# Kernel tuning notes

Hardware: AMD Instinct MI355X
Metric: run time of the kernel (lower is better)

## Reference

```python
import jax, jax.numpy as jnp
import numpy as np

N_VEH, N_PED = 16, 16
DV, DP = 40, 24            # vehicle / pedestrian slot obs dims
N = N_VEH + N_PED          # 32 agents
E, H = 128, 4              # embed_dim, num_heads
DH = E // H                # head_dim = 32
B = 4096
OBS = N_VEH * DV + N_PED * DP + N  # 1056


def setup_inputs() -> dict:
    key = jax.random.key(0)
    ks = jax.random.split(key, 12)
    s = lambda fan_in: 1.0 / np.sqrt(fan_in)
    inp = {
        "global_obs": jax.random.uniform(ks[0], (B, OBS), dtype=jnp.float32),
        # per-type projectors (stored as (in, out) so x @ W + b)
        "Wv": jax.random.uniform(ks[1], (DV, E), jnp.float32, -s(DV), s(DV)),
        "bv": jax.random.uniform(ks[2], (E,), jnp.float32, -s(DV), s(DV)),
        "Wp": jax.random.uniform(ks[3], (DP, E), jnp.float32, -s(DP), s(DP)),
        "bp": jax.random.uniform(ks[4], (E,), jnp.float32, -s(DP), s(DP)),
        # GAT layer 0 / 1: w (E, H*DH), a_src / a_dst (H, DH)
        "w0": jax.random.normal(ks[5], (E, H * DH), jnp.float32) * s(E),
        "asrc0": jax.random.normal(ks[6], (H, DH), jnp.float32) * s(DH),
        "adst0": jax.random.normal(ks[7], (H, DH), jnp.float32) * s(DH),
        "w1": jax.random.normal(ks[8], (E, H * DH), jnp.float32) * s(E),
        "asrc1": jax.random.normal(ks[9], (H, DH), jnp.float32) * s(DH),
        "adst1": jax.random.normal(ks[10], (H, DH), jnp.float32) * s(DH),
    }
    return inp


def _gat(x, alive, w, a_src, a_dst):
    # x: (B,N,E), alive: (B,N) in {0,1}
    b, n, _ = x.shape
    h = (x @ w).reshape(b, n, H, DH)                       # (B,N,H,DH)
    alpha_src = jnp.einsum("bnhd,hd->bnh", h, a_src)       # (B,N,H)
    alpha_dst = jnp.einsum("bnhd,hd->bnh", h, a_dst)
    e = alpha_src[:, :, None, :] + alpha_dst[:, None, :, :]  # (B,Ni,Nj,H)
    e = jnp.where(e > 0, e, 0.2 * e)                       # LeakyReLU(0.2)
    key_mask = alive[:, None, :, None] >= 0.5              # mask over j
    e = jnp.where(key_mask, e, -jnp.inf)
    attn = jax.nn.softmax(e, axis=2)                       # softmax over keys j
    attn = jnp.nan_to_num(attn)
    out = jnp.einsum("bijh,bjhd->bihd", attn, h)           # weighted aggregate
    return out.reshape(b, n, H * DH)                       # concat heads


def reference(global_obs, Wv, bv, Wp, bp, w0, asrc0, adst0, w1, asrc1, adst1):
    b = global_obs.shape[0]
    veh = global_obs[:, : N_VEH * DV].reshape(b, N_VEH, DV)
    ped = global_obs[:, N_VEH * DV : N_VEH * DV + N_PED * DP].reshape(b, N_PED, DP)
    alive_raw = global_obs[:, -N:]
    tokens = jnp.concatenate([veh @ Wv + bv, ped @ Wp + bp], axis=1)  # (B,N,E)
    alive = (alive_raw >= 0.5).astype(jnp.float32)
    all_dead = jnp.sum(alive, axis=1, keepdims=True) < 0.5
    alive = jnp.where(all_dead, jnp.ones_like(alive), alive)
    x = tokens
    for (w, a_s, a_d) in ((w0, asrc0, adst0), (w1, asrc1, adst1)):
        x = jax.nn.elu(_gat(x, alive, w, a_s, a_d))
    aw = alive[:, :, None]
    pooled = jnp.sum(x * aw, axis=1) / jnp.clip(jnp.sum(aw, axis=1), 1.0)
    return pooled
```

## Files before the change

kernel.cpp:

```cpp
#include <hip/hip_runtime.h>


#define NTOK 32
#define EMB  128
#define OBSL 1056
#define XSTR 136

typedef __attribute__((ext_vector_type(8))) short  short8;
typedef __attribute__((ext_vector_type(4))) float  floatx4;
typedef __attribute__((ext_vector_type(2))) unsigned uint2v;

__device__ __forceinline__ short f2bf(float f) {
  union { float f; unsigned u; } v; v.f = f;
  unsigned r = (v.u + 0x7fffu + ((v.u >> 16) & 1u)) >> 16;
  return (short)(unsigned short)r;
}
__device__ __forceinline__ unsigned pk2(float a, float b) {
  unsigned r; asm("v_cvt_pk_bf16_f32 %0, %1, %2" : "=v"(r) : "v"(a), "v"(b)); return r;
}
__device__ __forceinline__ float exp2_hw(float x) {
#if __has_builtin(__builtin_amdgcn_exp2f)
  return __builtin_amdgcn_exp2f(x);
#else
  return exp2f(x);
#endif
}
__device__ __forceinline__ float rcp_hw(float x) {
#if __has_builtin(__builtin_amdgcn_rcpf)
  return __builtin_amdgcn_rcpf(x);
#else
  return 1.0f / x;
#endif
}
__device__ __forceinline__ float elu1(float v) { return v > 0.f ? v : __expf(v) - 1.f; }
__device__ __forceinline__ floatx4 mfma16(short8 a, short8 b, floatx4 c) {
  return __builtin_amdgcn_mfma_f32_16x16x32_bf16(a, b, c, 0, 0, 0);
}

__global__ void prep_weights(const float* __restrict__ Wv, const float* __restrict__ Wp,
                             const float* __restrict__ w0, const float* __restrict__ w1,
                             short* __restrict__ ws) {
  int idx = blockIdx.x * 256 + threadIdx.x;
  if (idx < 8192) {
    int e = idx >> 6, k = idx & 63;
    float v = (k < 40) ? Wv[(size_t)k * EMB + e] : Wp[(size_t)(k - 40) * EMB + e];
    ws[idx] = f2bf(v);
  } else if (idx < 24576) {
    int t = idx - 8192; int e = t >> 7, k = t & 127;
    ws[idx] = f2bf(w0[(size_t)k * EMB + e]);
  } else {
    int t = idx - 24576; int e = t >> 7, k = t & 127;
    ws[idx] = f2bf(w1[(size_t)k * EMB + e]);
  }
}

__global__ __launch_bounds__(256, 4) void gnn_fused(
    const float* __restrict__ obs,
    const float* __restrict__ bv, const float* __restrict__ bp,
    const float* __restrict__ as0, const float* __restrict__ ad0,
    const float* __restrict__ as1, const float* __restrict__ ad1,
    const short* __restrict__ wsb,
    float* __restrict__ out)
{
  __shared__ __align__(16) short s_xh[EMB * XSTR];
  __shared__ float s_pool[4 * EMB];

  const int tid  = threadIdx.x;
  const int lane = tid & 63;
  const int wv   = tid >> 6;
  const int col  = lane & 15;
  const int quad = lane >> 4;
  const int b    = blockIdx.x * 4 + wv;

  const float* orow = obs + (size_t)b * OBSL;
  short* xbase = &s_xh[(wv * NTOK) * XSTR];
  const short8  z8 = {0,0,0,0,0,0,0,0};
  const floatx4 fz = {0.f,0.f,0.f,0.f};

  float flag; float invc;
  {
    float araw = (lane < NTOK) ? orow[1024 + lane] : 0.f;
    bool alv = (lane < NTOK) && (araw >= 0.5f);
    unsigned long long m = __ballot(alv);
    int cnt = __popcll(m);
    flag = alv ? 1.f : 0.f;
    if (cnt == 0) { flag = (lane < NTOK) ? 1.f : 0.f; cnt = NTOK; }
    invc = 1.f / (float)cnt;
  }
  float alv8[8];
  #pragma unroll
  for (int jj = 0; jj < 8; ++jj) alv8[jj] = __shfl(flag, quad * 8 + jj);
  const float alvI0 = __shfl(flag, col);
  const float alvI1 = __shfl(flag, 16 + col);

  #pragma unroll
  for (int it = 0; it < 4; ++it) {
    int c = it * 64 + lane;
    *(short8*)&xbase[(c >> 3) * XSTR + (c & 7) * 8] = z8;
  }
  #pragma unroll
  for (int it = 0; it < 4; ++it) {
    int i4 = it * 64 + lane;
    float4 v = *(const float4*)&orow[i4 * 4];
    int r, k;
    if (i4 < 160) { r = (i4 * 205) >> 11;  k = (i4 - r * 10) * 4; }
    else { int t2 = i4 - 160; int q6 = (t2 * 171) >> 10; r = 16 + q6; k = 40 + (t2 - q6 * 6) * 4; }
    uint2v u; u.x = pk2(v.x, v.y); u.y = pk2(v.z, v.w);
    *(uint2v*)&xbase[r * XSTR + k] = u;
  }

  {
    short8 Bxin[2][2];
    #pragma unroll
    for (int nt = 0; nt < 2; ++nt)
      #pragma unroll
      for (int kt = 0; kt < 2; ++kt)
        Bxin[nt][kt] = *(const short8*)&xbase[(nt * 16 + col) * XSTR + kt * 32 + quad * 8];
    const short* embT = wsb;
    #pragma unroll
    for (int mtE = 0; mtE < 8; ++mtE) {
      short8 A0 = *(const short8*)&embT[(mtE * 16 + col) * 64 + quad * 8];
      short8 A1 = *(const short8*)&embT[(mtE * 16 + col) * 64 + 32 + quad * 8];
      float4 bv4 = *(const float4*)&bv[mtE * 16 + quad * 4];
      float4 bp4 = *(const float4*)&bp[mtE * 16 + quad * 4];
      #pragma unroll
      for (int nt = 0; nt < 2; ++nt) {
        floatx4 acc = fz;
        acc = mfma16(A0, Bxin[nt][0], acc);
        acc = mfma16(A1, Bxin[nt][1], acc);
        float4 bb = nt ? bp4 : bv4;
        uint2v u; u.x = pk2(acc[0] + bb.x, acc[1] + bb.y); u.y = pk2(acc[2] + bb.z, acc[3] + bb.w);
        *(uint2v*)&xbase[(nt * 16 + col) * XSTR + mtE * 16 + quad * 4] = u;
      }
    }
  }

  for (int L = 0; L < 2; ++L) {
    const short* wT  = wsb + 8192 + L * 16384;
    const float* gas = L ? as1 : as0;
    const float* gad = L ? ad1 : ad0;

    short8 Bx[4][2];
    #pragma unroll
    for (int kt = 0; kt < 4; ++kt)
      #pragma unroll
      for (int nt = 0; nt < 2; ++nt)
        Bx[kt][nt] = *(const short8*)&xbase[(nt * 16 + col) * XSTR + kt * 32 + quad * 8];
    __syncthreads();

    float psrc[4][2], pdst[4][2];
    #pragma unroll
    for (int hh = 0; hh < 4; ++hh) { psrc[hh][0]=0.f; psrc[hh][1]=0.f; pdst[hh][0]=0.f; pdst[hh][1]=0.f; }
    #pragma unroll
    for (int g = 0; g < 2; ++g) {
      floatx4 acc[4][2];
      #pragma unroll
      for (int mi = 0; mi < 4; ++mi) { acc[mi][0] = fz; acc[mi][1] = fz; }
      #pragma unroll
      for (int mi = 0; mi < 4; ++mi) {
        const int mt = g * 4 + mi;
        const short* wrow = &wT[(mt * 16 + col) * 128 + quad * 8];
        short8 A0 = *(const short8*)&wrow[0];
        short8 A1 = *(const short8*)&wrow[32];
        short8 A2 = *(const short8*)&wrow[64];
        short8 A3 = *(const short8*)&wrow[96];
        #pragma unroll
        for (int nt = 0; nt < 2; ++nt) {
          acc[mi][nt] = mfma16(A0, Bx[0][nt], acc[mi][nt]);
          acc[mi][nt] = mfma16(A1, Bx[1][nt], acc[mi][nt]);
          acc[mi][nt] = mfma16(A2, Bx[2][nt], acc[mi][nt]);
          acc[mi][nt] = mfma16(A3, Bx[3][nt], acc[mi][nt]);
        }
      }
      #pragma unroll
      for (int mi = 0; mi < 4; ++mi) {
        const int mt = g * 4 + mi;
        const int hh = mt >> 1;
        float4 cs = *(const float4*)&gas[mt * 16 + quad * 4];
        float4 cd = *(const float4*)&gad[mt * 16 + quad * 4];
        #pragma unroll
        for (int nt = 0; nt < 2; ++nt) {
          floatx4 a = acc[mi][nt];
          psrc[hh][nt] += a[0]*cs.x + a[1]*cs.y + a[2]*cs.z + a[3]*cs.w;
          pdst[hh][nt] += a[0]*cd.x + a[1]*cd.y + a[2]*cd.z + a[3]*cd.w;
          unsigned u01 = pk2(a[0], a[1]);
          unsigned u23 = pk2(a[2], a[3]);
          unsigned short* hrow = (unsigned short*)&s_xh[(mt * 16 + quad * 4) * XSTR + wv * NTOK + nt * 16 + col];
          hrow[0]        = (unsigned short)u01;
          hrow[XSTR]     = (unsigned short)(u01 >> 16);
          hrow[2 * XSTR] = (unsigned short)u23;
          hrow[3 * XSTR] = (unsigned short)(u23 >> 16);
        }
      }
    }

    #pragma unroll
    for (int hh = 0; hh < 4; ++hh)
      #pragma unroll
      for (int nt = 0; nt < 2; ++nt) {
        float vs = psrc[hh][nt]; vs += __shfl_xor(vs, 16); vs += __shfl_xor(vs, 32);
        psrc[hh][nt] = vs * 1.44269504088896340736f;
        float vd = pdst[hh][nt]; vd += __shfl_xor(vd, 16); vd += __shfl_xor(vd, 32);
        pdst[hh][nt] = vd * 1.44269504088896340736f;
      }

    short8 pf[4][2];
    #pragma unroll
    for (int hh = 0; hh < 4; ++hh) {
      float vsel = (quad >> 1) ? pdst[hh][1] : pdst[hh][0];
      float ad8[8];
      #pragma unroll
      for (int jj = 0; jj < 8; ++jj) {
        float v = __shfl(vsel, ((quad >> 1) << 5) + ((quad & 1) << 3) + jj);
        ad8[jj] = (alv8[jj] >= 0.5f) ? v : -1e30f;
      }
      #pragma unroll
      for (int ii = 0; ii < 2; ++ii) {
        float ai = psrc[hh][ii];
        float ev[8]; float sum = 0.f;
        #pragma unroll
        for (int jj = 0; jj < 8; ++jj) {
          float e = ai + ad8[jj];
          e = fmaxf(e, 0.2f * e);
          float p = exp2_hw(e);
          ev[jj] = p; sum += p;
        }
        sum += __shfl_xor(sum, 16);
        sum += __shfl_xor(sum, 32);
        float inv = rcp_hw(sum);
        union { unsigned u4[4]; short8 s; } pu;
        #pragma unroll
        for (int p2 = 0; p2 < 4; ++p2) pu.u4[p2] = pk2(ev[2*p2] * inv, ev[2*p2+1] * inv);
        pf[hh][ii] = pu.s;
      }
    }

    short8 Ah[4][2];
    #pragma unroll
    for (int hh = 0; hh < 4; ++hh)
      #pragma unroll
      for (int mtE = 0; mtE < 2; ++mtE)
        Ah[hh][mtE] = *(const short8*)&s_xh[(hh * 32 + mtE * 16 + col) * XSTR + wv * NTOK + quad * 8];
    if (L == 0) __syncthreads();

    #pragma unroll
    for (int hh = 0; hh < 4; ++hh)
      #pragma unroll
      for (int mtE = 0; mtE < 2; ++mtE) {
        floatx4 po[2];
        #pragma unroll
        for (int nt = 0; nt < 2; ++nt) {
          po[nt] = mfma16(Ah[hh][mtE], pf[hh][nt], fz);
        }
        if (L == 0) {
          #pragma unroll
          for (int nt = 0; nt < 2; ++nt) {
            uint2v u;
            u.x = pk2(elu1(po[nt][0]), elu1(po[nt][1]));
            u.y = pk2(elu1(po[nt][2]), elu1(po[nt][3]));
            *(uint2v*)&xbase[(nt * 16 + col) * XSTR + hh * 32 + mtE * 16 + quad * 4] = u;
          }
        } else {
          #pragma unroll
          for (int r = 0; r < 4; ++r) {
            float s = elu1(po[0][r]) * alvI0 + elu1(po[1][r]) * alvI1;
            s += __shfl_xor(s, 1); s += __shfl_xor(s, 2);
            s += __shfl_xor(s, 4); s += __shfl_xor(s, 8);
            if (col == 0) s_pool[wv * EMB + hh * 32 + mtE * 16 + quad * 4 + r] = s;
          }
        }
      }
  }

  float r0 = s_pool[wv * EMB + lane];
  float r1 = s_pool[wv * EMB + 64 + lane];
  out[(size_t)b * EMB + lane]      = r0 * invc;
  out[(size_t)b * EMB + 64 + lane] = r1 * invc;
}

extern "C" void kernel_launch(void* const* d_in, const int* in_sizes, int n_in,
                              void* d_out, int out_size, void* d_ws, size_t ws_size,
                              hipStream_t stream) {
  const float* obs = (const float*)d_in[0];
  const float* Wv  = (const float*)d_in[1];
  const float* bv  = (const float*)d_in[2];
  const float* Wp  = (const float*)d_in[3];
  const float* bp  = (const float*)d_in[4];
  const float* w0  = (const float*)d_in[5];
  const float* as0 = (const float*)d_in[6];
  const float* ad0 = (const float*)d_in[7];
  const float* w1  = (const float*)d_in[8];
  const float* as1 = (const float*)d_in[9];
  const float* ad1 = (const float*)d_in[10];
  float* out = (float*)d_out;
  short* wsb = (short*)d_ws;

  int Bn = in_sizes[0] / OBSL;
  prep_weights<<<160, 256, 0, stream>>>(Wv, Wp, w0, w1, wsb);
  gnn_fused<<<Bn / 4, 256, 0, stream>>>(obs, bv, bp, as0, ad0, as1, ad1, wsb, out);
}
```

Baseline: 141.1 us.

## Split each batch item across two waves by head pairs and shrink LDS

Each batch item is now handled by two waves, and each wave computes two of the four attention heads. A block now covers two items instead of four, and the launch grid doubles. The per-wave h tile uses a compact stride in a smaller shared buffer, and launch bounds are raised to allow 8 blocks per CU for higher occupancy and lower per-wave latency. Pooled results are written straight to global memory from lane 0 of each group, which removes the s_pool staging. In exchange, extra block-wide barriers are needed to coordinate the two waves that share an item's x tile.

```diff
diff --git a/kernel.cpp b/kernel.cpp
--- a/kernel.cpp
+++ b/kernel.cpp
@@ -5,6 +5,8 @@
 #define EMB  128
 #define OBSL 1056
 #define XSTR 136
+#define HSTR 40
+#define TILE 5120
 
 typedef __attribute__((ext_vector_type(8))) short  short8;
 typedef __attribute__((ext_vector_type(4))) float  floatx4;
@@ -54,7 +56,7 @@
   }
 }
 
-__global__ __launch_bounds__(256, 4) void gnn_fused(
+__global__ __launch_bounds__(256, 8) void gnn_fused(
     const float* __restrict__ obs,
     const float* __restrict__ bv, const float* __restrict__ bp,
     const float* __restrict__ as0, const float* __restrict__ ad0,
@@ -62,18 +64,20 @@
     const short* __restrict__ wsb,
     float* __restrict__ out)
 {
-  __shared__ __align__(16) short s_xh[EMB * XSTR];
-  __shared__ float s_pool[4 * EMB];
+  __shared__ __align__(16) short s_t[2][TILE];
 
   const int tid  = threadIdx.x;
   const int lane = tid & 63;
   const int wv   = tid >> 6;
+  const int item = wv >> 1;
+  const int hw   = wv & 1;
   const int col  = lane & 15;
   const int quad = lane >> 4;
-  const int b    = blockIdx.x * 4 + wv;
+  const int b    = blockIdx.x * 2 + item;
 
   const float* orow = obs + (size_t)b * OBSL;
-  short* xbase = &s_xh[(wv * NTOK) * XSTR];
+  short* xbase = s_t[item];
+  short* hbase = &s_t[item][hw * 2560];
   const short8  z8 = {0,0,0,0,0,0,0,0};
   const floatx4 fz = {0.f,0.f,0.f,0.f};
 
@@ -87,20 +91,18 @@
     if (cnt == 0) { flag = (lane < NTOK) ? 1.f : 0.f; cnt = NTOK; }
     invc = 1.f / (float)cnt;
   }
-  float alv8[8];
-  #pragma unroll
-  for (int jj = 0; jj < 8; ++jj) alv8[jj] = __shfl(flag, quad * 8 + jj);
   const float alvI0 = __shfl(flag, col);
   const float alvI1 = __shfl(flag, 16 + col);
 
   #pragma unroll
-  for (int it = 0; it < 4; ++it) {
-    int c = it * 64 + lane;
+  for (int it = 0; it < 2; ++it) {
+    int c = (hw * 2 + it) * 64 + lane;
     *(short8*)&xbase[(c >> 3) * XSTR + (c & 7) * 8] = z8;
   }
+  __syncthreads();
   #pragma unroll
-  for (int it = 0; it < 4; ++it) {
-    int i4 = it * 64 + lane;
+  for (int it = 0; it < 2; ++it) {
+    int i4 = (hw * 2 + it) * 64 + lane;
     float4 v = *(const float4*)&orow[i4 * 4];
     int r, k;
     if (i4 < 160) { r = (i4 * 205) >> 11;  k = (i4 - r * 10) * 4; }
@@ -108,6 +110,7 @@
     uint2v u; u.x = pk2(v.x, v.y); u.y = pk2(v.z, v.w);
     *(uint2v*)&xbase[r * XSTR + k] = u;
   }
+  __syncthreads();
 
   {
     short8 Bxin[2][2];
@@ -116,9 +119,11 @@
       #pragma unroll
       for (int kt = 0; kt < 2; ++kt)
         Bxin[nt][kt] = *(const short8*)&xbase[(nt * 16 + col) * XSTR + kt * 32 + quad * 8];
+    __syncthreads();
     const short* embT = wsb;
     #pragma unroll
-    for (int mtE = 0; mtE < 8; ++mtE) {
+    for (int mi = 0; mi < 4; ++mi) {
+      const int mtE = hw * 4 + mi;
       short8 A0 = *(const short8*)&embT[(mtE * 16 + col) * 64 + quad * 8];
       short8 A1 = *(const short8*)&embT[(mtE * 16 + col) * 64 + 32 + quad * 8];
       float4 bv4 = *(const float4*)&bv[mtE * 16 + quad * 4];
@@ -140,6 +145,8 @@
     const float* gas = L ? as1 : as0;
     const float* gad = L ? ad1 : ad0;
 
+    __syncthreads();
+
     short8 Bx[4][2];
     #pragma unroll
     for (int kt = 0; kt < 4; ++kt)
@@ -148,17 +155,17 @@
         Bx[kt][nt] = *(const short8*)&xbase[(nt * 16 + col) * XSTR + kt * 32 + quad * 8];
     __syncthreads();
 
-    float psrc[4][2], pdst[4][2];
-    #pragma unroll
-    for (int hh = 0; hh < 4; ++hh) { psrc[hh][0]=0.f; psrc[hh][1]=0.f; pdst[hh][0]=0.f; pdst[hh][1]=0.f; }
+    float psrc[2][2], pdst[2][2];
+    #pragma unroll
+    for (int hl = 0; hl < 2; ++hl) { psrc[hl][0]=0.f; psrc[hl][1]=0.f; pdst[hl][0]=0.f; pdst[hl][1]=0.f; }
     #pragma unroll
     for (int g = 0; g < 2; ++g) {
-      floatx4 acc[4][2];
-      #pragma unroll
-      for (int mi = 0; mi < 4; ++mi) { acc[mi][0] = fz; acc[mi][1] = fz; }
-      #pragma unroll
-      for (int mi = 0; mi < 4; ++mi) {
-        const int mt = g * 4 + mi;
+      floatx4 acc[2][2];
+      #pragma unroll
+      for (int mi = 0; mi < 2; ++mi) { acc[mi][0] = fz; acc[mi][1] = fz; }
+      #pragma unroll
+      for (int mi = 0; mi < 2; ++mi) {
+        const int mt = hw * 4 + g * 2 + mi;
         const short* wrow = &wT[(mt * 16 + col) * 128 + quad * 8];
         short8 A0 = *(const short8*)&wrow[0];
         short8 A1 = *(const short8*)&wrow[32];
@@ -173,41 +180,45 @@
         }
       }
       #pragma unroll
-      for (int mi = 0; mi < 4; ++mi) {
-        const int mt = g * 4 + mi;
-        const int hh = mt >> 1;
+      for (int mi = 0; mi < 2; ++mi) {
+        const int mt = hw * 4 + g * 2 + mi;
         float4 cs = *(const float4*)&gas[mt * 16 + quad * 4];
         float4 cd = *(const float4*)&gad[mt * 16 + quad * 4];
+        const int rowloc = (g * 2 + mi) * 16 + quad * 4;
         #pragma unroll
         for (int nt = 0; nt < 2; ++nt) {
           floatx4 a = acc[mi][nt];
-          psrc[hh][nt] += a[0]*cs.x + a[1]*cs.y + a[2]*cs.z + a[3]*cs.w;
-          pdst[hh][nt] += a[0]*cd.x + a[1]*cd.y + a[2]*cd.z + a[3]*cd.w;
+          psrc[g][nt] += a[0]*cs.x + a[1]*cs.y + a[2]*cs.z + a[3]*cs.w;
+          pdst[g][nt] += a[0]*cd.x + a[1]*cd.y + a[2]*cd.z + a[3]*cd.w;
           unsigned u01 = pk2(a[0], a[1]);
           unsigned u23 = pk2(a[2], a[3]);
-          unsigned short* hrow = (unsigned short*)&s_xh[(mt * 16 + quad * 4) * XSTR + wv * NTOK + nt * 16 + col];
+          unsigned short* hrow = (unsigned short*)&hbase[rowloc * HSTR + nt * 16 + col];
           hrow[0]        = (unsigned short)u01;
-          hrow[XSTR]     = (unsigned short)(u01 >> 16);
-          hrow[2 * XSTR] = (unsigned short)u23;
-          hrow[3 * XSTR] = (unsigned short)(u23 >> 16);
+          hrow[HSTR]     = (unsigned short)(u01 >> 16);
+          hrow[2 * HSTR] = (unsigned short)u23;
+          hrow[3 * HSTR] = (unsigned short)(u23 >> 16);
         }
       }
     }
 
     #pragma unroll
-    for (int hh = 0; hh < 4; ++hh)
+    for (int hl = 0; hl < 2; ++hl)
       #pragma unroll
       for (int nt = 0; nt < 2; ++nt) {
-        float vs = psrc[hh][nt]; vs += __shfl_xor(vs, 16); vs += __shfl_xor(vs, 32);
-        psrc[hh][nt] = vs * 1.44269504088896340736f;
-        float vd = pdst[hh][nt]; vd += __shfl_xor(vd, 16); vd += __shfl_xor(vd, 32);
-        pdst[hh][nt] = vd * 1.44269504088896340736f;
-      }
-
-    short8 pf[4][2];
-    #pragma unroll
-    for (int hh = 0; hh < 4; ++hh) {
-      float vsel = (quad >> 1) ? pdst[hh][1] : pdst[hh][0];
+        float vs = psrc[hl][nt]; vs += __shfl_xor(vs, 16); vs += __shfl_xor(vs, 32);
+        psrc[hl][nt] = vs * 1.44269504088896340736f;
+        float vd = pdst[hl][nt]; vd += __shfl_xor(vd, 16); vd += __shfl_xor(vd, 32);
+        pdst[hl][nt] = vd * 1.44269504088896340736f;
+      }
+
+    float alv8[8];
+    #pragma unroll
+    for (int jj = 0; jj < 8; ++jj) alv8[jj] = __shfl(flag, quad * 8 + jj);
+
+    short8 pf[2][2];
+    #pragma unroll
+    for (int hl = 0; hl < 2; ++hl) {
+      float vsel = (quad >> 1) ? pdst[hl][1] : pdst[hl][0];
       float ad8[8];
       #pragma unroll
       for (int jj = 0; jj < 8; ++jj) {
@@ -216,7 +227,7 @@
       }
       #pragma unroll
       for (int ii = 0; ii < 2; ++ii) {
-        float ai = psrc[hh][ii];
+        float ai = psrc[hl][ii];
         float ev[8]; float sum = 0.f;
         #pragma unroll
         for (int jj = 0; jj < 8; ++jj) {
@@ -231,34 +242,35 @@
         union { unsigned u4[4]; short8 s; } pu;
         #pragma unroll
         for (int p2 = 0; p2 < 4; ++p2) pu.u4[p2] = pk2(ev[2*p2] * inv, ev[2*p2+1] * inv);
-        pf[hh][ii] = pu.s;
+        pf[hl][ii] = pu.s;
       }
     }
 
-    short8 Ah[4][2];
-    #pragma unroll
-    for (int hh = 0; hh < 4; ++hh)
-      #pragma unroll
-      for (int mtE = 0; mtE < 2; ++mtE)
-        Ah[hh][mtE] = *(const short8*)&s_xh[(hh * 32 + mtE * 16 + col) * XSTR + wv * NTOK + quad * 8];
+    short8 Ah[2][2];
+    #pragma unroll
+    for (int hl = 0; hl < 2; ++hl)
+      #pragma unroll
+      for (int mt2 = 0; mt2 < 2; ++mt2)
+        Ah[hl][mt2] = *(const short8*)&hbase[(hl * 32 + mt2 * 16 + col) * HSTR + quad * 8];
     if (L == 0) __syncthreads();
 
     #pragma unroll
-    for (int hh = 0; hh < 4; ++hh)
-      #pragma unroll
-      for (int mtE = 0; mtE < 2; ++mtE) {
+    for (int hl = 0; hl < 2; ++hl)
+      #pragma unroll
+      for (int mt2 = 0; mt2 < 2; ++mt2) {
         floatx4 po[2];
         #pragma unroll
         for (int nt = 0; nt < 2; ++nt) {
-          po[nt] = mfma16(Ah[hh][mtE], pf[hh][nt], fz);
-        }
+          po[nt] = mfma16(Ah[hl][mt2], pf[hl][nt], fz);
+        }
+        const int ecol = hw * 64 + hl * 32 + mt2 * 16 + quad * 4;
         if (L == 0) {
           #pragma unroll
           for (int nt = 0; nt < 2; ++nt) {
             uint2v u;
             u.x = pk2(elu1(po[nt][0]), elu1(po[nt][1]));
             u.y = pk2(elu1(po[nt][2]), elu1(po[nt][3]));
-            *(uint2v*)&xbase[(nt * 16 + col) * XSTR + hh * 32 + mtE * 16 + quad * 4] = u;
+            *(uint2v*)&xbase[(nt * 16 + col) * XSTR + ecol] = u;
           }
         } else {
           #pragma unroll
@@ -266,16 +278,11 @@
             float s = elu1(po[0][r]) * alvI0 + elu1(po[1][r]) * alvI1;
             s += __shfl_xor(s, 1); s += __shfl_xor(s, 2);
             s += __shfl_xor(s, 4); s += __shfl_xor(s, 8);
-            if (col == 0) s_pool[wv * EMB + hh * 32 + mtE * 16 + quad * 4 + r] = s;
+            if (col == 0) out[(size_t)b * EMB + ecol + r] = s * invc;
           }
         }
       }
   }
-
-  float r0 = s_pool[wv * EMB + lane];
-  float r1 = s_pool[wv * EMB + 64 + lane];
-  out[(size_t)b * EMB + lane]      = r0 * invc;
-  out[(size_t)b * EMB + 64 + lane] = r1 * invc;
 }
 
 extern "C" void kernel_launch(void* const* d_in, const int* in_sizes, int n_in,
@@ -297,5 +304,5 @@
 
   int Bn = in_sizes[0] / OBSL;
   prep_weights<<<160, 256, 0, stream>>>(Wv, Wp, w0, w1, wsb);
-  gnn_fused<<<Bn / 4, 256, 0, stream>>>(obs, bv, bp, as0, ad0, as1, ad1, wsb, out);
-}
+  gnn_fused<<<Bn / 2, 256, 0, stream>>>(obs, bv, bp, as0, ad0, as1, ad1, wsb, out);
+}
```

New measurement: 160.6 us. 1.14x slower.
